# Performance work log

Hardware: AMD Instinct MI355X
Metric: run time of the kernel (lower is better)

Reference implementation:

```python
import jax, jax.numpy as jnp
import numpy as np
import math

N_WAY, K_SHOT, Q_QUERY, PRJ_NUM, D = 5, 5, 15, 6, 64


def setup_inputs() -> dict:
    key = jax.random.key(0)
    k1, k2 = jax.random.split(key)
    feat = jax.random.normal(k1, (600, 64, 10, 10), dtype=jnp.float32)
    label = jax.random.randint(k2, (450,), 0, N_WAY)
    scale = jnp.ones((1,), dtype=jnp.float32)
    r = jnp.zeros((2,), dtype=jnp.float32)
    return {"feat": feat, "label": label, "scale": scale, "r": r}


def reference(feat, label, scale, r):
    ns = N_WAY * K_SHOT * PRJ_NUM  # 150 support images
    inv_sqrt_d = 1.0 / math.sqrt(D)
    support_xf = feat[:ns] * inv_sqrt_d
    query_xf = feat[ns:] * inv_sqrt_d
    q, c, h, w = query_xf.shape

    # support: (n_way, k_shot*prj_num*h*w, c)
    support = support_xf.reshape(N_WAY, K_SHOT * PRJ_NUM, c, h * w)
    support = jnp.transpose(support, (0, 1, 3, 2)).reshape(N_WAY, -1, c)
    # query: (q*h*w, c)
    query = jnp.transpose(query_xf.reshape(q, c, h * w), (0, 2, 1)).reshape(q * h * w, c)

    alpha, beta = r[0], r[1]
    reg = support.shape[1] / support.shape[2]
    lam = reg * jnp.exp(alpha)
    rho = jnp.exp(beta)

    # Woodbury / normal-equations path: hat = (S^T S + lam I)^-1 S^T S, per class
    sts = jnp.einsum('nkc,nkd->ncd', support, support)  # (n_way, c, c)
    m = sts + lam * jnp.eye(c, dtype=sts.dtype)[None]
    hat = jnp.linalg.inv(m) @ sts  # (n_way, c, c)

    Q_bar = jnp.einsum('qc,ncd->nqd', query, hat) * rho  # (n_way, q*h*w, c)
    dist = jnp.sum((Q_bar - query[None]) ** 2, axis=2).T  # (q*h*w, n_way)
    neg_l2_dist = -dist.reshape(q, h * w, N_WAY).mean(axis=1)  # (q, n_way)

    y_pred = jax.nn.softmax(neg_l2_dist, axis=1)
    logits = neg_l2_dist * scale[0]
    logp = jax.nn.log_softmax(logits, axis=1)
    loss = -jnp.mean(jnp.take_along_axis(logp, label[:, None], axis=1))
    return y_pred, loss
```

## Files before the change

### kernel.cpp

```cpp
#include <hip/hip_runtime.h>
#include <math.h>


typedef __attribute__((ext_vector_type(8))) short short8;
typedef __attribute__((ext_vector_type(4))) short short4v;
typedef __attribute__((ext_vector_type(4))) float f32x4;

#define NSUP 150
#define NQ 450
#define PIX 100
#define IMG_STRIDE 6400
#define MAGIC 0x5F3D2B1Cu

static __device__ __forceinline__ short bf16r(float x) {
  unsigned u = __builtin_bit_cast(unsigned, x);
  u += 0x7FFFu + ((u >> 16) & 1u);
  return (short)(u >> 16);
}
static __device__ __forceinline__ float b2f(short v) {
  return __builtin_bit_cast(float, ((unsigned)(unsigned short)v) << 16);
}
static __device__ __forceinline__ void st_flag(unsigned* p, unsigned v) {
  __builtin_amdgcn_fence(__ATOMIC_RELEASE, "agent");
  __hip_atomic_store(p, v, __ATOMIC_RELAXED, __HIP_MEMORY_SCOPE_AGENT);
}
static __device__ __forceinline__ void spin_rlx(unsigned* p) {
  int guard = 1 << 22;
  while (__hip_atomic_load(p, __ATOMIC_RELAXED, __HIP_MEMORY_SCOPE_AGENT) != MAGIC
         && --guard) __builtin_amdgcn_s_sleep(2);
}

static __device__ __forceinline__ void gram_accum(const float* __restrict__ f,
                                                  f32x4 acc[4][4], int r, int g) {
  #pragma unroll
  for (int ks = 0; ks < 4; ++ks) {
    short8 frag[4];
    const int kb = ks * 32 + g * 8;
    #pragma unroll
    for (int R = 0; R < 4; ++R) {
      short8 q;
      const float* p = f + (R * 16 + r) * PIX + kb;
      if (ks < 3) {
        float4 lo = *(const float4*)p;
        float4 hi = *(const float4*)(p + 4);
        q[0] = bf16r(lo.x); q[1] = bf16r(lo.y); q[2] = bf16r(lo.z); q[3] = bf16r(lo.w);
        q[4] = bf16r(hi.x); q[5] = bf16r(hi.y); q[6] = bf16r(hi.z); q[7] = bf16r(hi.w);
      } else if (g == 0) {
        float4 lo = *(const float4*)p;
        q[0] = bf16r(lo.x); q[1] = bf16r(lo.y); q[2] = bf16r(lo.z); q[3] = bf16r(lo.w);
        q[4] = 0; q[5] = 0; q[6] = 0; q[7] = 0;
      } else {
        #pragma unroll
        for (int j = 0; j < 8; ++j) q[j] = 0;
      }
      frag[R] = q;
    }
    #pragma unroll
    for (int R = 0; R < 4; ++R)
      #pragma unroll
      for (int C = 0; C < 4; ++C)
        acc[R][C] = __builtin_amdgcn_mfma_f32_16x16x32_bf16(frag[R], frag[C],
                                                            acc[R][C], 0, 0, 0);
  }
}

static __device__ __forceinline__ void mm64q(const short* A, const short* B,
                                             f32x4 t[2][2], int r, int g,
                                             int wr, int wc) {
  #pragma unroll
  for (int ks = 0; ks < 2; ++ks) {
    short8 af[2], bfr[2];
    #pragma unroll
    for (int i = 0; i < 2; ++i) {
      af[i]  = *(const short8*)(A + (wr * 32 + i * 16 + r) * 72 + ks * 32 + g * 8);
      bfr[i] = *(const short8*)(B + (wc * 32 + i * 16 + r) * 72 + ks * 32 + g * 8);
    }
    #pragma unroll
    for (int i = 0; i < 2; ++i)
      #pragma unroll
      for (int j = 0; j < 2; ++j)
        t[i][j] = __builtin_amdgcn_mfma_f32_16x16x32_bf16(af[i], bfr[j],
                                                          t[i][j], 0, 0, 0);
  }
}

#define ZERO_ACC4(t)                                  \
  _Pragma("unroll") for (int R = 0; R < 4; ++R)       \
  _Pragma("unroll") for (int C = 0; C < 4; ++C)       \
  _Pragma("unroll") for (int q = 0; q < 4; ++q) t[R][C][q] = 0.f;

#define ZERO_ACC2(t)                                  \
  _Pragma("unroll") for (int R = 0; R < 2; ++R)       \
  _Pragma("unroll") for (int C = 0; C < 2; ++C)       \
  _Pragma("unroll") for (int q = 0; q < 4; ++q) t[R][C][q] = 0.f;

__global__ __launch_bounds__(256) void k_fused(
    const float* __restrict__ feat, const int* __restrict__ label,
    const float* __restrict__ scale, const float* __restrict__ rvec,
    float* __restrict__ out,
    float* __restrict__ partial,
    unsigned short* __restrict__ Gneg,
    float* __restrict__ blockloss,
    unsigned* __restrict__ gflag,
    unsigned* __restrict__ sflag,
    unsigned* __restrict__ lflag) {
  __shared__ __align__(16) char smem[65536];
  const int b = blockIdx.x, tid = threadIdx.x;
  const int wave = tid >> 6, lane = tid & 63;
  const int r = lane & 15, g = lane >> 4;

  if (b < 30) {
    float (*gbuf)[4096] = (float (*)[4096])smem;
    const int cls = b / 6, jb = b % 6;
    const int ks = wave, kb = ks * 32 + g * 8;
    f32x4 acc[4][4];
    ZERO_ACC4(acc)
    for (int im = 0; im < 5; ++im) {
      const float* f = feat + (size_t)(cls * 30 + jb * 5 + im) * IMG_STRIDE;
      short8 frag[4];
      #pragma unroll
      for (int R = 0; R < 4; ++R) {
        short8 q;
        const float* p = f + (R * 16 + r) * PIX + kb;
        if (ks < 3) {
          float4 lo = *(const float4*)p;
          float4 hi = *(const float4*)(p + 4);
          q[0] = bf16r(lo.x); q[1] = bf16r(lo.y); q[2] = bf16r(lo.z); q[3] = bf16r(lo.w);
          q[4] = bf16r(hi.x); q[5] = bf16r(hi.y); q[6] = bf16r(hi.z); q[7] = bf16r(hi.w);
        } else if (g == 0) {
          float4 lo = *(const float4*)p;
          q[0] = bf16r(lo.x); q[1] = bf16r(lo.y); q[2] = bf16r(lo.z); q[3] = bf16r(lo.w);
          q[4] = 0; q[5] = 0; q[6] = 0; q[7] = 0;
        } else {
          #pragma unroll
          for (int j = 0; j < 8; ++j) q[j] = 0;
        }
        frag[R] = q;
      }
      #pragma unroll
      for (int R = 0; R < 4; ++R)
        #pragma unroll
        for (int C = 0; C < 4; ++C)
          acc[R][C] = __builtin_amdgcn_mfma_f32_16x16x32_bf16(frag[R], frag[C],
                                                              acc[R][C], 0, 0, 0);
    }
    #pragma unroll
    for (int R = 0; R < 4; ++R)
      #pragma unroll
      for (int C = 0; C < 4; ++C)
        #pragma unroll
        for (int q = 0; q < 4; ++q) {
          const int row = R * 16 + g * 4 + q, col = C * 16 + r;
          gbuf[wave][row * 64 + col] = acc[R][C][q];
        }
    __syncthreads();
    float* outp = partial + (size_t)b * 4096;
    for (int c = tid; c < 1024; c += 256) {
      f32x4 s0 = *(const f32x4*)&gbuf[0][4 * c];
      f32x4 s1 = *(const f32x4*)&gbuf[1][4 * c];
      f32x4 s2 = *(const f32x4*)&gbuf[2][4 * c];
      f32x4 s3 = *(const f32x4*)&gbuf[3][4 * c];
      f32x4 s = s0 + s1 + s2 + s3;
      *(float4*)(outp + 4 * c) = *(float4*)&s;
    }
    __syncthreads();
    if (tid == 0) st_flag(&gflag[b], MAGIC);
    if (b >= 5) return;

    float* Ms   = (float*)(smem);
    short* Mb   = (short*)(smem + 16640);
    short* Tb   = (short*)(smem + 25856);
    short* Xa   = (short*)(smem + 35072);
    short* Xc   = (short*)(smem + 44288);
    float* radp = (float*)(smem + 53504);
    float* scal = (float*)(smem + 54528);

    const int n = b;
    const int wr = wave >> 1, wc = wave & 1;
    const float lam = 46.875f * expf(rvec[0]);
    const float rho = expf(rvec[1]);

    if (tid < 6) spin_rlx(&gflag[6 * n + tid]);
    __syncthreads();
    __builtin_amdgcn_fence(__ATOMIC_ACQUIRE, "agent");

    {
      const float* base = partial + (size_t)n * 6 * 4096;
      for (int c = tid; c < 1024; c += 256) {
        float4 s = {0.f, 0.f, 0.f, 0.f};
        #pragma unroll
        for (int p = 0; p < 6; ++p) {
          float4 v = *(const float4*)(base + p * 4096 + 4 * c);
          s.x += v.x; s.y += v.y; s.z += v.z; s.w += v.w;
        }
        const int e = 4 * c, row = e >> 6, col = e & 63;
        Ms[row * 65 + col + 0] = s.x * (1.f / 64.f);
        Ms[row * 65 + col + 1] = s.y * (1.f / 64.f);
        Ms[row * 65 + col + 2] = s.z * (1.f / 64.f);
        Ms[row * 65 + col + 3] = s.w * (1.f / 64.f);
      }
    }
    __syncthreads();
    if (tid < 64) Ms[tid * 65 + tid] += lam;
    __syncthreads();

    {
      const int row = tid & 63, part = tid >> 6;
      float s = 0.f;
      #pragma unroll
      for (int k = 0; k < 16; ++k) s += fabsf(Ms[row * 65 + part * 16 + k]);
      radp[part * 64 + row] = s;
    }
    __syncthreads();
    if (tid < 64) {
      const float diag = Ms[tid * 65 + tid];
      const float rad = radp[tid] + radp[64 + tid] + radp[128 + tid] +
                        radp[192 + tid] - fabsf(diag);
      float lo = diag - rad, hi = diag + rad;
      for (int off = 32; off; off >>= 1) {
        lo = fminf(lo, __shfl_down(lo, off));
        hi = fmaxf(hi, __shfl_down(hi, off));
      }
      if (tid == 0) {
        const float a = fmaxf(lo, lam);
        const float bb = hi;
        const float s = a + bb, d = bb - a;
        scal[0] = s;
        scal[1] = 8.f / (2.f * s * s - d * d);
      }
    }
    __syncthreads();
    const float s0 = scal[0], theta = scal[1];

    for (int e = tid; e < 4096; e += 256) {
      const int i = e >> 6, j = e & 63;
      const float m = Ms[i * 65 + j];
      Mb[i * 72 + j] = bf16r(m);
      Xa[i * 72 + j] = bf16r(theta * (((i == j) ? s0 : 0.f) - m));
    }
    __syncthreads();

    short* x = Xa;
    short* xn = Xc;
    for (int it = 0; it < 2; ++it) {
      {
        f32x4 t[2][2];
        ZERO_ACC2(t)
        mm64q(x, Mb, t, r, g, wr, wc);
        #pragma unroll
        for (int i = 0; i < 2; ++i)
          #pragma unroll
          for (int j = 0; j < 2; ++j)
            #pragma unroll
            for (int q = 0; q < 4; ++q) {
              const int row = wr * 32 + i * 16 + g * 4 + q;
              const int col = wc * 32 + j * 16 + r;
              Tb[row * 72 + col] = bf16r(t[i][j][q]);
            }
      }
      __syncthreads();
      {
        f32x4 t[2][2];
        ZERO_ACC2(t)
        mm64q(Tb, x, t, r, g, wr, wc);
        #pragma unroll
        for (int i = 0; i < 2; ++i)
          #pragma unroll
          for (int j = 0; j < 2; ++j)
            #pragma unroll
            for (int q = 0; q < 4; ++q) {
              const int row = wr * 32 + i * 16 + g * 4 + q;
              const int col = wc * 32 + j * 16 + r;
              const int idx = row * 72 + col;
              xn[idx] = bf16r(2.f * b2f(x[idx]) - t[i][j][q]);
            }
      }
      __syncthreads();
      short* tmp = x; x = xn; xn = tmp;
    }

    for (int e = tid; e < 4096; e += 256) {
      const int i = e >> 6, j = e & 63;
      const float xv = b2f(x[i * 72 + j]);
      Tb[i * 72 + j] = bf16r(((i == j) ? (rho - 1.f) : 0.f) - rho * lam * xv);
    }
    __syncthreads();

    {
      f32x4 t[2][2];
      ZERO_ACC2(t)
      mm64q(Tb, Tb, t, r, g, wr, wc);
      #pragma unroll
      for (int i = 0; i < 2; ++i)
        #pragma unroll
        for (int j = 0; j < 2; ++j)
          #pragma unroll
          for (int q = 0; q < 4; ++q) {
            const int row = wr * 32 + i * 16 + g * 4 + q;
            const int col = wc * 32 + j * 16 + r;
            Gneg[n * 4096 + row * 64 + col] =
                (unsigned short)bf16r(t[i][j][q] * (-0.01f));
          }
    }
    __syncthreads();
    if (tid == 0) st_flag(&sflag[n], MAGIC);
    return;
  }

  const int img = (b - 30) * 4 + wave;
  const bool ok = img < NQ;
  f32x4 acc[4][4];
  ZERO_ACC4(acc)
  if (ok)
    gram_accum(feat + (size_t)(NSUP + img) * IMG_STRIDE, acc, r, g);

  if (tid < 5) spin_rlx(&sflag[tid]);
  __syncthreads();
  __builtin_amdgcn_fence(__ATOMIC_ACQUIRE, "agent");

  unsigned short* Gs = (unsigned short*)smem;
  for (int e = tid; e < 5120; e += 256) {
    const int e4 = e * 4;
    const int nn = e4 >> 12, rem = e4 & 4095, row = rem >> 6, col = rem & 63;
    *(short4v*)&Gs[nn * 4352 + row * 68 + col] = *(const short4v*)&Gneg[e4];
  }
  __syncthreads();

  float myloss = 0.f;
  float nl[5] = {0.f, 0.f, 0.f, 0.f, 0.f};
  if (ok) {
    #pragma unroll
    for (int R = 0; R < 4; ++R)
      #pragma unroll
      for (int C = 0; C < 4; ++C)
        #pragma unroll
        for (int q = 0; q < 4; ++q) {
          const int row = R * 16 + g * 4 + q, col = C * 16 + r;
          const float cv = acc[R][C][q] * (1.f / 64.f);
          const int idx = row * 68 + col;
          #pragma unroll
          for (int nn = 0; nn < 5; ++nn)
            nl[nn] += b2f((short)Gs[nn * 4352 + idx]) * cv;
        }
    #pragma unroll
    for (int nn = 0; nn < 5; ++nn)
      for (int off = 32; off; off >>= 1) nl[nn] += __shfl_down(nl[nn], off);

    if (lane == 0) {
      float mx = nl[0];
      #pragma unroll
      for (int nn = 1; nn < 5; ++nn) mx = fmaxf(mx, nl[nn]);
      float ex[5], se = 0.f;
      #pragma unroll
      for (int nn = 0; nn < 5; ++nn) { ex[nn] = expf(nl[nn] - mx); se += ex[nn]; }
      const float inv = 1.f / se;
      #pragma unroll
      for (int nn = 0; nn < 5; ++nn) out[img * 5 + nn] = ex[nn] * inv;

      const float sc = scale[0];
      float mx2 = nl[0] * sc;
      #pragma unroll
      for (int nn = 1; nn < 5; ++nn) mx2 = fmaxf(mx2, nl[nn] * sc);
      float se2 = 0.f;
      #pragma unroll
      for (int nn = 0; nn < 5; ++nn) se2 += expf(nl[nn] * sc - mx2);
      myloss = mx2 + logf(se2) - nl[label[img]] * sc;
    }
  }

  float* wl = (float*)(smem + 43584);
  if (lane == 0) wl[wave] = ok ? myloss : 0.f;
  __syncthreads();
  if (tid == 0) {
    blockloss[b - 30] = wl[0] + wl[1] + wl[2] + wl[3];
    st_flag(&lflag[b - 30], MAGIC);
  }

  if (b == 30 && wave == 0) {
    for (int i = lane; i < 113; i += 64) spin_rlx(&lflag[i]);
    __builtin_amdgcn_fence(__ATOMIC_ACQUIRE, "agent");
    float s = 0.f;
    for (int i = lane; i < 113; i += 64) s += blockloss[i];
    for (int off = 32; off; off >>= 1) s += __shfl_down(s, off);
    if (lane == 0) out[2250] = s / 450.f;
  }
}

extern "C" void kernel_launch(void* const* d_in, const int* in_sizes, int n_in,
                              void* d_out, int out_size, void* d_ws, size_t ws_size,
                              hipStream_t stream) {
  const float* feat  = (const float*)d_in[0];
  const int*   label = (const int*)d_in[1];
  const float* scale = (const float*)d_in[2];
  const float* rvec  = (const float*)d_in[3];
  float* out = (float*)d_out;

  char* ws = (char*)d_ws;
  float*          partial   = (float*)ws;
  unsigned short* Gneg      = (unsigned short*)(ws + 491520);
  float*          blockloss = (float*)(ws + 532480);
  unsigned*       flags     = (unsigned*)(ws + 532992);
  unsigned* gflag = flags;
  unsigned* sflag = flags + 32;
  unsigned* lflag = flags + 64;

  k_fused<<<dim3(143), dim3(256), 0, stream>>>(feat, label, scale, rvec, out,
                                               partial, Gneg, blockloss,
                                               gflag, sflag, lflag);
}
```

Measured before the change: 24.40 us.

## Move solver to dedicated blocks and process two query images per wave

The five per-class solver blocks become separate blocks 30-34 instead of reusing gram blocks 0-4. This lets the gram blocks exit right after publishing their partials. Query blocks now handle 8 images each, two per wave, which cuts the grid from 143 to 92 blocks and the loss-reduction fan-in from 113 to 57 flags. The intent is less launch and sync overhead, in exchange for doubled accumulator registers per wave and serialized per-wave query gram work.

After: 28.71 us. 17.7% more time.

```diff
diff --git a/kernel.cpp b/kernel.cpp
--- a/kernel.cpp
+++ b/kernel.cpp
@@ -82,6 +82,29 @@
         t[i][j] = __builtin_amdgcn_mfma_f32_16x16x32_bf16(af[i], bfr[j],
                                                           t[i][j], 0, 0, 0);
   }
+}
+
+static __device__ __forceinline__ void dot5(const f32x4 acc[4][4],
+                                            const unsigned short* Gs,
+                                            int r, int g, float nl[5]) {
+  #pragma unroll
+  for (int nn = 0; nn < 5; ++nn) nl[nn] = 0.f;
+  #pragma unroll
+  for (int R = 0; R < 4; ++R)
+    #pragma unroll
+    for (int C = 0; C < 4; ++C)
+      #pragma unroll
+      for (int q = 0; q < 4; ++q) {
+        const int row = R * 16 + g * 4 + q, col = C * 16 + r;
+        const float cv = acc[R][C][q] * (1.f / 64.f);
+        const int idx = row * 68 + col;
+        #pragma unroll
+        for (int nn = 0; nn < 5; ++nn)
+          nl[nn] += b2f((short)Gs[nn * 4352 + idx]) * cv;
+      }
+  #pragma unroll
+  for (int nn = 0; nn < 5; ++nn)
+    for (int off = 32; off; off >>= 1) nl[nn] += __shfl_down(nl[nn], off);
 }
 
 #define ZERO_ACC4(t)                                  \
@@ -165,8 +188,10 @@
     }
     __syncthreads();
     if (tid == 0) st_flag(&gflag[b], MAGIC);
-    if (b >= 5) return;
-
+    return;
+  }
+
+  if (b < 35) {
     float* Ms   = (float*)(smem);
     short* Mb   = (short*)(smem + 16640);
     short* Tb   = (short*)(smem + 25856);
@@ -175,7 +200,7 @@
     float* radp = (float*)(smem + 53504);
     float* scal = (float*)(smem + 54528);
 
-    const int n = b;
+    const int n = b - 30;
     const int wr = wave >> 1, wc = wave & 1;
     const float lam = 46.875f * expf(rvec[0]);
     const float rho = expf(rvec[1]);
@@ -307,12 +332,17 @@
     return;
   }
 
-  const int img = (b - 30) * 4 + wave;
-  const bool ok = img < NQ;
-  f32x4 acc[4][4];
-  ZERO_ACC4(acc)
-  if (ok)
-    gram_accum(feat + (size_t)(NSUP + img) * IMG_STRIDE, acc, r, g);
+  const int qb = b - 35;
+  const int base = qb * 8;
+  const int imgA = base + wave, imgB = base + 4 + wave;
+  const bool okA = imgA < NQ, okB = imgB < NQ;
+  f32x4 accA[4][4], accB[4][4];
+  ZERO_ACC4(accA)
+  ZERO_ACC4(accB)
+  if (okA)
+    gram_accum(feat + (size_t)(NSUP + imgA) * IMG_STRIDE, accA, r, g);
+  if (okB)
+    gram_accum(feat + (size_t)(NSUP + imgB) * IMG_STRIDE, accB, r, g);
 
   if (tid < 5) spin_rlx(&sflag[tid]);
   __syncthreads();
@@ -326,61 +356,51 @@
   }
   __syncthreads();
 
-  float myloss = 0.f;
-  float nl[5] = {0.f, 0.f, 0.f, 0.f, 0.f};
-  if (ok) {
-    #pragma unroll
-    for (int R = 0; R < 4; ++R)
-      #pragma unroll
-      for (int C = 0; C < 4; ++C)
-        #pragma unroll
-        for (int q = 0; q < 4; ++q) {
-          const int row = R * 16 + g * 4 + q, col = C * 16 + r;
-          const float cv = acc[R][C][q] * (1.f / 64.f);
-          const int idx = row * 68 + col;
-          #pragma unroll
-          for (int nn = 0; nn < 5; ++nn)
-            nl[nn] += b2f((short)Gs[nn * 4352 + idx]) * cv;
-        }
-    #pragma unroll
-    for (int nn = 0; nn < 5; ++nn)
-      for (int off = 32; off; off >>= 1) nl[nn] += __shfl_down(nl[nn], off);
-
-    if (lane == 0) {
-      float mx = nl[0];
-      #pragma unroll
-      for (int nn = 1; nn < 5; ++nn) mx = fmaxf(mx, nl[nn]);
-      float ex[5], se = 0.f;
-      #pragma unroll
-      for (int nn = 0; nn < 5; ++nn) { ex[nn] = expf(nl[nn] - mx); se += ex[nn]; }
-      const float inv = 1.f / se;
-      #pragma unroll
-      for (int nn = 0; nn < 5; ++nn) out[img * 5 + nn] = ex[nn] * inv;
-
-      const float sc = scale[0];
-      float mx2 = nl[0] * sc;
-      #pragma unroll
-      for (int nn = 1; nn < 5; ++nn) mx2 = fmaxf(mx2, nl[nn] * sc);
-      float se2 = 0.f;
-      #pragma unroll
-      for (int nn = 0; nn < 5; ++nn) se2 += expf(nl[nn] * sc - mx2);
-      myloss = mx2 + logf(se2) - nl[label[img]] * sc;
-    }
-  }
-
   float* wl = (float*)(smem + 43584);
-  if (lane == 0) wl[wave] = ok ? myloss : 0.f;
+  const float sc = scale[0];
+  for (int h = 0; h < 2; ++h) {
+    const bool ok = h ? okB : okA;
+    const int img = h ? imgB : imgA;
+    if (ok) {
+      float nl[5];
+      dot5(h ? accB : accA, Gs, r, g, nl);
+      if (lane == 0) {
+        float mx = nl[0];
+        #pragma unroll
+        for (int nn = 1; nn < 5; ++nn) mx = fmaxf(mx, nl[nn]);
+        float ex[5], se = 0.f;
+        #pragma unroll
+        for (int nn = 0; nn < 5; ++nn) { ex[nn] = expf(nl[nn] - mx); se += ex[nn]; }
+        const float inv = 1.f / se;
+        #pragma unroll
+        for (int nn = 0; nn < 5; ++nn) out[img * 5 + nn] = ex[nn] * inv;
+
+        float mx2 = nl[0] * sc;
+        #pragma unroll
+        for (int nn = 1; nn < 5; ++nn) mx2 = fmaxf(mx2, nl[nn] * sc);
+        float se2 = 0.f;
+        #pragma unroll
+        for (int nn = 0; nn < 5; ++nn) se2 += expf(nl[nn] * sc - mx2);
+        wl[wave * 2 + h] = mx2 + logf(se2) - nl[label[img]] * sc;
+      }
+    } else if (lane == 0) {
+      wl[wave * 2 + h] = 0.f;
+    }
+  }
   __syncthreads();
   if (tid == 0) {
-    blockloss[b - 30] = wl[0] + wl[1] + wl[2] + wl[3];
-    st_flag(&lflag[b - 30], MAGIC);
-  }
-
-  if (b == 30 && wave == 0) {
-    for (int i = lane; i < 113; i += 64) spin_rlx(&lflag[i]);
+    float s = 0.f;
+    #pragma unroll
+    for (int i = 0; i < 8; ++i) s += wl[i];
+    blockloss[qb] = s;
+    st_flag(&lflag[qb], MAGIC);
+  }
+
+  if (qb == 0 && wave == 0) {
+    for (int i = lane; i < 57; i += 64) spin_rlx(&lflag[i]);
     __builtin_amdgcn_fence(__ATOMIC_ACQUIRE, "agent");
     float s = 0.f;
-    for (int i = lane; i < 113; i += 64) s += blockloss[i];
+    for (int i = lane; i < 57; i += 64) s += blockloss[i];
     for (int off = 32; off; off >>= 1) s += __shfl_down(s, off);
     if (lane == 0) out[2250] = s / 450.f;
   }
@@ -404,7 +424,7 @@
   unsigned* sflag = flags + 32;
   unsigned* lflag = flags + 64;
 
-  k_fused<<<dim3(143), dim3(256), 0, stream>>>(feat, label, scale, rvec, out,
-                                               partial, Gneg, blockloss,
-                                               gflag, sflag, lflag);
-}
+  k_fused<<<dim3(92), dim3(256), 0, stream>>>(feat, label, scale, rvec, out,
+                                              partial, Gneg, blockloss,
+                                              gflag, sflag, lflag);
+}
```
